# Performance work log

Measured on AMD Instinct MI355X. Metric: run time of the kernel, lower is better.

Reference implementation:

```python
import jax, jax.numpy as jnp
import numpy as np

NUM_EXPERTS = 8
TOP_K = 2
N_EMBD = 1024
B, T = 4, 2048


def setup_inputs() -> dict:
    key = jax.random.key(0)
    k_x, k_g, k_e = jax.random.split(key, 3)
    x = jax.random.normal(k_x, (B, T, N_EMBD), dtype=jnp.float32)
    # torch nn.Linear weight layout: (out_features, in_features); y = x @ W.T
    scale = 1.0 / np.sqrt(N_EMBD)
    gate_w = jax.random.uniform(k_g, (NUM_EXPERTS, N_EMBD), dtype=jnp.float32,
                                minval=-scale, maxval=scale)
    expert_w = jax.random.uniform(k_e, (NUM_EXPERTS, N_EMBD, N_EMBD), dtype=jnp.float32,
                                  minval=-scale, maxval=scale)
    return {"x": x, "gate_w": gate_w, "expert_w": expert_w}


def reference(x, gate_w, expert_w):
    Bb, Tt, C = x.shape
    xf = x.reshape(Bb * Tt, C)                        # (N, C)
    logits = xf @ gate_w.T                            # (N, E)
    w, sel = jax.lax.top_k(logits, TOP_K)             # (N, K) each
    # softmax over the selected logits in float32, cast back (matches torch)
    w = jax.nn.softmax(w.astype(jnp.float32), axis=1).astype(xf.dtype)
    # scatter per-token routing weights into a dense (N, E) combine matrix
    n = xf.shape[0]
    w_full = jnp.zeros((n, NUM_EXPERTS), dtype=xf.dtype)
    w_full = w_full.at[jnp.arange(n)[:, None], sel].add(w)
    # all-expert outputs: y_e = x @ W_e.T  -> (N, E, C)
    expert_out = jnp.einsum('nc,edc->ned', xf, expert_w)
    out = jnp.einsum('ne,ned->nd', w_full, expert_out)  # combine
    return out.reshape(Bb, Tt, C)
```

## Files before the change

### kernel.cpp

```cpp
#include <hip/hip_runtime.h>
#include <hip/hip_bf16.h>

#define NEXP 8
#define NEMB 1024
#define NTOK 8192
#define BM 128
#define BN 128
#define BK 64
#define NK  (NEMB / BK)
#define RBS 24
#define BLD_STRIPE 512

typedef __attribute__((ext_vector_type(8))) short  bf16x8;
typedef __attribute__((ext_vector_type(8))) unsigned short u16x8;
typedef __attribute__((ext_vector_type(4))) float  f32x4;

#define XB_BYTES   (NTOK * NEMB * 2)
#define WB_BYTES   (NEXP * NEMB * NEMB * 2)
#define CNT_OFF    (XB_BYTES + WB_BYTES)
#define LTOK_OFF   (CNT_OFF + 256)
#define LWT_OFF    (LTOK_OFF + NEXP * NTOK * 4)
#define SELW_OFF   (LWT_OFF + NEXP * NTOK * 4)
#define META_OFF   (SELW_OFF + NTOK * 16)

__device__ __forceinline__ unsigned short f2bf(float f) {
    unsigned u = __builtin_bit_cast(unsigned, f);
    unsigned r = (u + 0x7fffu + ((u >> 16) & 1u)) >> 16;
    return (unsigned short)r;
}

__global__ void k_cvt_w(const float* __restrict__ w, unsigned short* __restrict__ wb) {
    int i = (blockIdx.x * blockDim.x + threadIdx.x) * 8;
    f32x4 v0 = *reinterpret_cast<const f32x4*>(w + i);
    f32x4 v1 = *reinterpret_cast<const f32x4*>(w + i + 4);
    u16x8 o;
#pragma unroll
    for (int j = 0; j < 4; ++j) { o[j] = f2bf(v0[j]); o[4 + j] = f2bf(v1[j]); }
    *reinterpret_cast<u16x8*>(wb + i) = o;
}

__global__ __launch_bounds__(256)
void k_gate(const float* __restrict__ x, const float* __restrict__ gw,
            unsigned short* __restrict__ xb, int4* __restrict__ selw) {
    int t = threadIdx.x, wave = t >> 6, lane = t & 63;
    int n = blockIdx.x * 4 + wave;

    const float* xr = x + (size_t)n * NEMB + lane * 16;
    f32x4 xv[4];
#pragma unroll
    for (int j = 0; j < 4; ++j) xv[j] = *reinterpret_cast<const f32x4*>(xr + j * 4);

    u16x8 o0, o1;
#pragma unroll
    for (int q = 0; q < 4; ++q) {
        o0[q] = f2bf(xv[0][q]); o0[4 + q] = f2bf(xv[1][q]);
        o1[q] = f2bf(xv[2][q]); o1[4 + q] = f2bf(xv[3][q]);
    }
    u16x8* xo = reinterpret_cast<u16x8*>(xb + (size_t)n * NEMB + lane * 16);
    xo[0] = o0; xo[1] = o1;

    float p[NEXP];
#pragma unroll
    for (int e = 0; e < NEXP; ++e) {
        const float* gr = gw + e * NEMB + lane * 16;
        f32x4 a = xv[0] * *reinterpret_cast<const f32x4*>(gr);
#pragma unroll
        for (int j = 1; j < 4; ++j) a += xv[j] * *reinterpret_cast<const f32x4*>(gr + j * 4);
        p[e] = a[0] + a[1] + a[2] + a[3];
    }
#pragma unroll
    for (int e = 0; e < NEXP; ++e) {
        float v = p[e];
#pragma unroll
        for (int m = 1; m < 64; m <<= 1) v += __shfl_xor(v, m, 64);
        p[e] = v;
    }
    if (lane == 0) {
        int e0 = 0; float b0 = p[0];
#pragma unroll
        for (int e = 1; e < NEXP; ++e) if (p[e] > b0) { b0 = p[e]; e0 = e; }
        int e1 = -1; float b1 = -3.4e38f;
#pragma unroll
        for (int e = 0; e < NEXP; ++e) if (e != e0 && p[e] > b1) { b1 = p[e]; e1 = e; }
        float ex = __expf(b1 - b0);
        float inv = 1.f / (1.f + ex);
        int4 s;
        s.x = e0; s.y = e1;
        s.z = __float_as_int(inv); s.w = __float_as_int(ex * inv);
        selw[n] = s;
    }
}

__global__ __launch_bounds__(256)
void k_build(const int4* __restrict__ selw, int* __restrict__ counts,
             int* __restrict__ ltok, float* __restrict__ lwt) {
    int e = blockIdx.y;
    int n0 = blockIdx.x * BLD_STRIPE;
    __shared__ int lcnt, base;
    __shared__ int   toks[BLD_STRIPE];
    __shared__ float wts[BLD_STRIPE];
    if (threadIdx.x == 0) lcnt = 0;
    __syncthreads();
    for (int i = threadIdx.x; i < BLD_STRIPE; i += 256) {
        int4 s = selw[n0 + i];
        if (s.x == e) {
            int p = atomicAdd(&lcnt, 1);
            toks[p] = n0 + i; wts[p] = __int_as_float(s.z);
        }
        if (s.y == e) {
            int p = atomicAdd(&lcnt, 1);
            toks[p] = n0 + i; wts[p] = __int_as_float(s.w);
        }
    }
    __syncthreads();
    if (threadIdx.x == 0) base = atomicAdd(&counts[e], lcnt);
    __syncthreads();
    for (int i = threadIdx.x; i < lcnt; i += 256) {
        ltok[e * NTOK + base + i] = toks[i];
        lwt[e * NTOK + base + i]  = wts[i];
    }
}

__global__ void k_padW(const int* __restrict__ counts, int* __restrict__ ltok,
                       float* __restrict__ lwt, int* __restrict__ meta) {
    __shared__ int nt[NEXP];
    int t = threadIdx.x;
    if (t < NEXP) {
        nt[t] = (counts[t] + BM - 1) / BM;
        meta[1 + t] = nt[t];
    }
    __syncthreads();
    for (int e = 0; e < NEXP; ++e) {
        int c = counts[e], cp = nt[e] * BM;
        for (int i = c + t; i < cp; i += 256) {
            ltok[e * NTOK + i] = -1;
            lwt[e * NTOK + i]  = 0.f;
        }
    }
}

__global__ __launch_bounds__(256)
void k_gemm(const unsigned short* __restrict__ xb, const unsigned short* __restrict__ wb,
            const int* __restrict__ ltok, const float* __restrict__ lwt,
            const int* __restrict__ meta, float* __restrict__ out) {
    int b  = blockIdx.x;
    int e  = b & 7;
    int j  = b >> 3;
    int cb = j & 7;
    int rb = j >> 3;
    if (rb >= meta[1 + e]) return;

    __shared__ unsigned short As[BM * BK];
    __shared__ unsigned short Bs[BN * BK];
    __shared__ int   tokS[BM];
    __shared__ float wS[BM];

    int t = threadIdx.x, lane = t & 63, wave = t >> 6;
    int wr = wave >> 1, wc = wave & 1;
    int fr = lane & 15, fq = lane >> 4, fs = fr & 7;

    if (t < BM) {
        tokS[t] = ltok[e * NTOK + rb * BM + t];
        wS[t]   = lwt[e * NTOK + rb * BM + t];
    }

    const unsigned short* aSrc[4];
    const unsigned short* bSrc[4];
    int ldsOff[4];
#pragma unroll
    for (int i = 0; i < 4; ++i) {
        int idx = i * 256 + t;
        int r   = idx >> 3;
        int csw = (idx & 7) ^ (r & 7);
        int tok = ltok[e * NTOK + rb * BM + r];
        int tokc = tok < 0 ? 0 : tok;
        aSrc[i] = xb + (size_t)tokc * NEMB + csw * 8;
        bSrc[i] = wb + (size_t)e * NEMB * NEMB + (size_t)(cb * BN + r) * NEMB + csw * 8;
        ldsOff[i] = (i * 256 + wave * 64) * 8;
    }

    f32x4 acc[4][4];
#pragma unroll
    for (int m = 0; m < 4; ++m)
#pragma unroll
        for (int n = 0; n < 4; ++n) acc[m][n] = (f32x4){0.f, 0.f, 0.f, 0.f};

    for (int kk = 0; kk < NK; ++kk) {
#pragma unroll
        for (int i = 0; i < 4; ++i) {
            __builtin_amdgcn_global_load_lds(
                (const __attribute__((address_space(1))) void*)(aSrc[i] + kk * BK),
                (__attribute__((address_space(3))) void*)(As + ldsOff[i]), 16, 0, 0);
            __builtin_amdgcn_global_load_lds(
                (const __attribute__((address_space(1))) void*)(bSrc[i] + kk * BK),
                (__attribute__((address_space(3))) void*)(Bs + ldsOff[i]), 16, 0, 0);
        }
        __syncthreads();

#pragma unroll
        for (int ks = 0; ks < 2; ++ks) {
            int ch = (fq + 4 * ks) ^ fs;
            bf16x8 af[4], bfr[4];
#pragma unroll
            for (int m = 0; m < 4; ++m)
                af[m] = *reinterpret_cast<const bf16x8*>(
                    As + (wr * 64 + m * 16 + fr) * BK + ch * 8);
#pragma unroll
            for (int n = 0; n < 4; ++n)
                bfr[n] = *reinterpret_cast<const bf16x8*>(
                    Bs + (wc * 64 + n * 16 + fr) * BK + ch * 8);
            __builtin_amdgcn_s_setprio(1);
#pragma unroll
            for (int m = 0; m < 4; ++m)
#pragma unroll
                for (int n = 0; n < 4; ++n)
                    acc[m][n] = __builtin_amdgcn_mfma_f32_16x16x32_bf16(
                        af[m], bfr[n], acc[m][n], 0, 0, 0);
            __builtin_amdgcn_s_setprio(0);
        }
        __syncthreads();
    }

#pragma unroll
    for (int m = 0; m < 4; ++m) {
#pragma unroll
        for (int jj = 0; jj < 4; ++jj) {
            int row = wr * 64 + m * 16 + fq * 4 + jj;
            int tok = tokS[row];
            if (tok < 0) continue;
            float wgt = wS[row];
            float* orow = out + (size_t)tok * NEMB + cb * BN + wc * 64 + fr;
#pragma unroll
            for (int n = 0; n < 4; ++n)
                unsafeAtomicAdd(orow + n * 16, wgt * acc[m][n][jj]);
        }
    }
}

extern "C" void kernel_launch(void* const* d_in, const int* in_sizes, int n_in,
                              void* d_out, int out_size, void* d_ws, size_t ws_size,
                              hipStream_t stream) {
    const float* x  = (const float*)d_in[0];
    const float* gw = (const float*)d_in[1];
    const float* ew = (const float*)d_in[2];
    float* out = (float*)d_out;

    char* ws = (char*)d_ws;
    unsigned short* xb = (unsigned short*)(ws);
    unsigned short* wb = (unsigned short*)(ws + XB_BYTES);
    int*   counts = (int*)(ws + CNT_OFF);
    int*   ltok   = (int*)(ws + LTOK_OFF);
    float* lwt    = (float*)(ws + LWT_OFF);
    int4*  selw   = (int4*)(ws + SELW_OFF);
    int*   meta   = (int*)(ws + META_OFF);

    hipMemsetAsync(counts, 0, 8 * sizeof(int), stream);
    hipMemsetAsync(out, 0, (size_t)NTOK * NEMB * sizeof(float), stream);

    k_cvt_w<<<4096, 256, 0, stream>>>(ew, wb);
    k_gate<<<NTOK / 4, 256, 0, stream>>>(x, gw, xb, selw);
    k_build<<<dim3(NTOK / BLD_STRIPE, NEXP), 256, 0, stream>>>(selw, counts, ltok, lwt);
    k_padW<<<1, 256, 0, stream>>>(counts, ltok, lwt, meta);
    k_gemm<<<8 * 8 * RBS, 256, 0, stream>>>(xb, wb, ltok, lwt, meta, out);
}
```

Before: 137.7 us.

## Enlarge expert GEMM tiles to 256x256 with split-K and fuse prep kernels

The expert GEMM moves from 128x128 tiles with 4 waves to 256x256 tiles with 8 waves. K is split in two halves across blocks, and partial sums are merged through the existing atomic adds. Each block does more MFMA work per LDS load and the grid stays large enough to fill the device. In exchange, each output element gets twice as many atomics, LDS use per block rises to about 64KB, and more rows are padded per expert. The weight-conversion kernel and the gate kernel are also merged into one launch to save launch overhead.

```diff
diff --git a/kernel.cpp b/kernel.cpp
--- a/kernel.cpp
+++ b/kernel.cpp
@@ -4,11 +4,10 @@
 #define NEXP 8
 #define NEMB 1024
 #define NTOK 8192
-#define BM 128
-#define BN 128
+#define BM 256
+#define BN 256
 #define BK 64
-#define NK  (NEMB / BK)
-#define RBS 24
+#define RBS 12
 #define BLD_STRIPE 512
 
 typedef __attribute__((ext_vector_type(8))) short  bf16x8;
@@ -29,21 +28,22 @@
     return (unsigned short)r;
 }
 
-__global__ void k_cvt_w(const float* __restrict__ w, unsigned short* __restrict__ wb) {
-    int i = (blockIdx.x * blockDim.x + threadIdx.x) * 8;
-    f32x4 v0 = *reinterpret_cast<const f32x4*>(w + i);
-    f32x4 v1 = *reinterpret_cast<const f32x4*>(w + i + 4);
-    u16x8 o;
-#pragma unroll
-    for (int j = 0; j < 4; ++j) { o[j] = f2bf(v0[j]); o[4 + j] = f2bf(v1[j]); }
-    *reinterpret_cast<u16x8*>(wb + i) = o;
-}
-
 __global__ __launch_bounds__(256)
-void k_gate(const float* __restrict__ x, const float* __restrict__ gw,
+void k_prep(const float* __restrict__ x, const float* __restrict__ gw,
+            const float* __restrict__ ew, unsigned short* __restrict__ wb,
             unsigned short* __restrict__ xb, int4* __restrict__ selw) {
+    if (blockIdx.x < 4096) {
+        int i = (blockIdx.x * 256 + threadIdx.x) * 8;
+        f32x4 v0 = *reinterpret_cast<const f32x4*>(ew + i);
+        f32x4 v1 = *reinterpret_cast<const f32x4*>(ew + i + 4);
+        u16x8 o;
+#pragma unroll
+        for (int j = 0; j < 4; ++j) { o[j] = f2bf(v0[j]); o[4 + j] = f2bf(v1[j]); }
+        *reinterpret_cast<u16x8*>(wb + i) = o;
+        return;
+    }
     int t = threadIdx.x, wave = t >> 6, lane = t & 63;
-    int n = blockIdx.x * 4 + wave;
+    int n = (blockIdx.x - 4096) * 4 + wave;
 
     const float* xr = x + (size_t)n * NEMB + lane * 16;
     f32x4 xv[4];
@@ -139,16 +139,18 @@
     }
 }
 
-__global__ __launch_bounds__(256)
+__global__ __launch_bounds__(512, 2)
 void k_gemm(const unsigned short* __restrict__ xb, const unsigned short* __restrict__ wb,
             const int* __restrict__ ltok, const float* __restrict__ lwt,
             const int* __restrict__ meta, float* __restrict__ out) {
     int b  = blockIdx.x;
     int e  = b & 7;
     int j  = b >> 3;
-    int cb = j & 7;
+    int kh = j & 1;
+    int cb = (j >> 1) & 3;
     int rb = j >> 3;
     if (rb >= meta[1 + e]) return;
+    int kB = kh * 8;
 
     __shared__ unsigned short As[BM * BK];
     __shared__ unsigned short Bs[BN * BK];
@@ -156,12 +158,12 @@
     __shared__ float wS[BM];
 
     int t = threadIdx.x, lane = t & 63, wave = t >> 6;
-    int wr = wave >> 1, wc = wave & 1;
+    int wr = wave >> 2, wc = wave & 3;
     int fr = lane & 15, fq = lane >> 4, fs = fr & 7;
 
-    if (t < BM) {
-        tokS[t] = ltok[e * NTOK + rb * BM + t];
-        wS[t]   = lwt[e * NTOK + rb * BM + t];
+    for (int i = t; i < BM; i += 512) {
+        tokS[i] = ltok[e * NTOK + rb * BM + i];
+        wS[i]   = lwt[e * NTOK + rb * BM + i];
     }
 
     const unsigned short* aSrc[4];
@@ -169,30 +171,31 @@
     int ldsOff[4];
 #pragma unroll
     for (int i = 0; i < 4; ++i) {
-        int idx = i * 256 + t;
+        int idx = i * 512 + t;
         int r   = idx >> 3;
         int csw = (idx & 7) ^ (r & 7);
         int tok = ltok[e * NTOK + rb * BM + r];
         int tokc = tok < 0 ? 0 : tok;
         aSrc[i] = xb + (size_t)tokc * NEMB + csw * 8;
         bSrc[i] = wb + (size_t)e * NEMB * NEMB + (size_t)(cb * BN + r) * NEMB + csw * 8;
-        ldsOff[i] = (i * 256 + wave * 64) * 8;
-    }
-
-    f32x4 acc[4][4];
-#pragma unroll
-    for (int m = 0; m < 4; ++m)
+        ldsOff[i] = (i * 512 + wave * 64) * 8;
+    }
+
+    f32x4 acc[8][4];
+#pragma unroll
+    for (int m = 0; m < 8; ++m)
 #pragma unroll
         for (int n = 0; n < 4; ++n) acc[m][n] = (f32x4){0.f, 0.f, 0.f, 0.f};
 
-    for (int kk = 0; kk < NK; ++kk) {
+    for (int kt = 0; kt < 8; ++kt) {
+        int ko = (kB + kt) * BK;
 #pragma unroll
         for (int i = 0; i < 4; ++i) {
             __builtin_amdgcn_global_load_lds(
-                (const __attribute__((address_space(1))) void*)(aSrc[i] + kk * BK),
+                (const __attribute__((address_space(1))) void*)(aSrc[i] + ko),
                 (__attribute__((address_space(3))) void*)(As + ldsOff[i]), 16, 0, 0);
             __builtin_amdgcn_global_load_lds(
-                (const __attribute__((address_space(1))) void*)(bSrc[i] + kk * BK),
+                (const __attribute__((address_space(1))) void*)(bSrc[i] + ko),
                 (__attribute__((address_space(3))) void*)(Bs + ldsOff[i]), 16, 0, 0);
         }
         __syncthreads();
@@ -200,18 +203,18 @@
 #pragma unroll
         for (int ks = 0; ks < 2; ++ks) {
             int ch = (fq + 4 * ks) ^ fs;
-            bf16x8 af[4], bfr[4];
-#pragma unroll
-            for (int m = 0; m < 4; ++m)
+            bf16x8 af[8], bfr[4];
+#pragma unroll
+            for (int m = 0; m < 8; ++m)
                 af[m] = *reinterpret_cast<const bf16x8*>(
-                    As + (wr * 64 + m * 16 + fr) * BK + ch * 8);
+                    As + (wr * 128 + m * 16 + fr) * BK + ch * 8);
 #pragma unroll
             for (int n = 0; n < 4; ++n)
                 bfr[n] = *reinterpret_cast<const bf16x8*>(
                     Bs + (wc * 64 + n * 16 + fr) * BK + ch * 8);
             __builtin_amdgcn_s_setprio(1);
 #pragma unroll
-            for (int m = 0; m < 4; ++m)
+            for (int m = 0; m < 8; ++m)
 #pragma unroll
                 for (int n = 0; n < 4; ++n)
                     acc[m][n] = __builtin_amdgcn_mfma_f32_16x16x32_bf16(
@@ -222,10 +225,10 @@
     }
 
 #pragma unroll
-    for (int m = 0; m < 4; ++m) {
+    for (int m = 0; m < 8; ++m) {
 #pragma unroll
         for (int jj = 0; jj < 4; ++jj) {
-            int row = wr * 64 + m * 16 + fq * 4 + jj;
+            int row = wr * 128 + m * 16 + fq * 4 + jj;
             int tok = tokS[row];
             if (tok < 0) continue;
             float wgt = wS[row];
@@ -257,9 +260,8 @@
     hipMemsetAsync(counts, 0, 8 * sizeof(int), stream);
     hipMemsetAsync(out, 0, (size_t)NTOK * NEMB * sizeof(float), stream);
 
-    k_cvt_w<<<4096, 256, 0, stream>>>(ew, wb);
-    k_gate<<<NTOK / 4, 256, 0, stream>>>(x, gw, xb, selw);
+    k_prep<<<4096 + NTOK / 4, 256, 0, stream>>>(x, gw, ew, wb, xb, selw);
     k_build<<<dim3(NTOK / BLD_STRIPE, NEXP), 256, 0, stream>>>(selw, counts, ltok, lwt);
     k_padW<<<1, 256, 0, stream>>>(counts, ltok, lwt, meta);
-    k_gemm<<<8 * 8 * RBS, 256, 0, stream>>>(xb, wb, ltok, lwt, meta, out);
-}
+    k_gemm<<<8 * RBS * 4 * 2, 512, 0, stream>>>(xb, wb, ltok, lwt, meta, out);
+}
```

Result: slower. 196.1 us (+42.4%).
